# Kernel optimization log

Hardware: AMD Instinct MI355X
Metric: run time of the kernel (lower is better)

## Reference

```python
import jax, jax.numpy as jnp
import numpy as np

N = 100000       # nodes
E = 1600000      # edges
F_IN = 128       # num_node_features
H = 256          # graph_hidden_channels
NHID = 512
NOUT = 256
G = 256          # graphs in batch


def setup_inputs() -> dict:
    key = jax.random.key(0)
    ks = jax.random.split(key, 14)
    x = jax.random.normal(ks[0], (N, F_IN), jnp.float32)
    src = jax.random.randint(ks[1], (E,), 0, N, jnp.int32)
    dst = jax.random.randint(ks[2], (E,), 0, N, jnp.int32)
    batch = jnp.sort(jax.random.randint(ks[3], (N,), 0, G, jnp.int32))
    def lin(k, fan_in, fan_out):
        return jax.random.normal(k, (fan_in, fan_out), jnp.float32) * (1.0 / np.sqrt(fan_in))
    return {
        "x": x, "src": src, "dst": dst, "batch": batch,
        "W1": lin(ks[4], F_IN, H), "b1": jnp.zeros((H,), jnp.float32),
        "W2": lin(ks[5], H, H),    "b2": jnp.zeros((H,), jnp.float32),
        "W3": lin(ks[6], H, H),    "b3": jnp.zeros((H,), jnp.float32),
        "Wm1": lin(ks[7], H, NHID), "bm1": jnp.zeros((NHID,), jnp.float32),
        "Wm2": lin(ks[8], NHID, NOUT), "bm2": jnp.zeros((NOUT,), jnp.float32),
    }


def _gcn_layer(h_in, W, b, src, dst, dinv):
    # GCNConv: transform, then symmetric-normalized aggregation with self-loops.
    h = h_in @ W                                            # [N, out]
    norm = (dinv[src] * dinv[dst])[:, None]                 # [E, 1]
    agg = jax.ops.segment_sum(h[src] * norm, dst, num_segments=N)
    agg = agg + h * (dinv * dinv)[:, None]                  # self-loop term (norm = 1/deg)
    return agg + b


def reference(x, src, dst, batch, W1, b1, W2, b2, W3, b3, Wm1, bm1, Wm2, bm2):
    # degrees include the added self-loop (+1)
    deg = 1.0 + jax.ops.segment_sum(jnp.ones((E,), x.dtype), dst, num_segments=N)
    dinv = jax.lax.rsqrt(deg)                               # deg^{-1/2}

    h = jax.nn.relu(_gcn_layer(x, W1, b1, src, dst, dinv))
    h = jax.nn.relu(_gcn_layer(h, W2, b2, src, dst, dinv))
    h = _gcn_layer(h, W3, b3, src, dst, dinv)               # no relu before pooling

    # global mean pool over graphs
    counts = jax.ops.segment_sum(jnp.ones((N,), x.dtype), batch, num_segments=G)
    pooled = jax.ops.segment_sum(h, batch, num_segments=G) / jnp.maximum(counts, 1.0)[:, None]

    out = jax.nn.relu(pooled @ Wm1 + bm1) @ Wm2 + bm2       # [G, NOUT]
    return out
```

## Files before the change

kernel.cpp:

```cpp
#include <hip/hip_runtime.h>
#include <hip/hip_bf16.h>

#define N_NODES 100000
#define N_EDGES 1600000
#define F_IN    128
#define H       256
#define NHID    512
#define NOUT    256
#define G_GR    256

typedef unsigned short u16;
typedef __attribute__((ext_vector_type(8))) short s16x8;
typedef __attribute__((ext_vector_type(8))) unsigned short u16x8;
typedef __attribute__((ext_vector_type(4))) float f32x4;

__device__ __forceinline__ float bf2f(u16 u) {
    union { unsigned int i; float f; } v; v.i = ((unsigned int)u) << 16; return v.f;
}
__device__ __forceinline__ u16 f2bf(float f) {
    union { float f; unsigned int i; } v; v.f = f;
    unsigned int x = v.i;
    x += 0x7fffu + ((x >> 16) & 1u);
    return (u16)(x >> 16);
}

#define CD_BLKS   1563
#define SPX_BLKS  ((N_NODES * F_IN) / 1024)
#define T1_BLKS   ((F_IN * H) / 256)
#define T2_BLKS   ((H * H) / 256)
#define T3_BLKS   ((H * H) / 256)
#define TM1_BLKS  ((H * NHID) / 256)
#define TM2_BLKS  ((NHID * NOUT) / 256)
#define HEAD_BLKS (CD_BLKS + SPX_BLKS + T1_BLKS + T2_BLKS + T3_BLKS + TM1_BLKS + TM2_BLKS + 2)

__device__ __forceinline__ void transpose_split_body(const float* __restrict__ W,
        u16* __restrict__ thi, u16* __restrict__ tlo, int K, int N, int id) {
    int n = id / K, k = id - n * K;
    float f = W[(size_t)k * N + n];
    u16 h = f2bf(f);
    thi[id] = h;
    tlo[id] = f2bf(f - bf2f(h));
}

__global__ __launch_bounds__(256) void prep_head(
        const int* __restrict__ dst, int* __restrict__ degc,
        const float* __restrict__ x, u16* __restrict__ x_bf,
        const float* __restrict__ W1, u16* __restrict__ t1h, u16* __restrict__ t1l,
        const float* __restrict__ W2, u16* __restrict__ t2h, u16* __restrict__ t2l,
        const float* __restrict__ W3, u16* __restrict__ t3h, u16* __restrict__ t3l,
        const float* __restrict__ Wm1, u16* __restrict__ tm1h, u16* __restrict__ tm1l,
        const float* __restrict__ Wm2, u16* __restrict__ tm2h, u16* __restrict__ tm2l,
        const int* __restrict__ batch, int* __restrict__ goff) {
    int bid = blockIdx.x;
    if (bid < CD_BLKS) {
        int base = bid * 1024 + threadIdx.x;
#pragma unroll
        for (int q = 0; q < 4; q++) {
            int e = base + q * 256;
            if (e < N_EDGES) atomicAdd(&degc[dst[e]], 1);
        }
        return;
    }
    bid -= CD_BLKS;
    if (bid < SPX_BLKS) {
        int idx = bid * 256 + threadIdx.x;
        float4 f = *(const float4*)&x[(size_t)idx * 4];
        ushort4 o;
        o.x = f2bf(f.x); o.y = f2bf(f.y); o.z = f2bf(f.z); o.w = f2bf(f.w);
        *(ushort4*)&x_bf[(size_t)idx * 4] = o;
        return;
    }
    bid -= SPX_BLKS;
    if (bid < T1_BLKS) {
        transpose_split_body(W1, t1h, t1l, F_IN, H, bid * 256 + threadIdx.x);
        return;
    }
    bid -= T1_BLKS;
    if (bid < T2_BLKS) {
        transpose_split_body(W2, t2h, t2l, H, H, bid * 256 + threadIdx.x);
        return;
    }
    bid -= T2_BLKS;
    if (bid < T3_BLKS) {
        transpose_split_body(W3, t3h, t3l, H, H, bid * 256 + threadIdx.x);
        return;
    }
    bid -= T3_BLKS;
    if (bid < TM1_BLKS) {
        transpose_split_body(Wm1, tm1h, tm1l, H, NHID, bid * 256 + threadIdx.x);
        return;
    }
    bid -= TM1_BLKS;
    if (bid < TM2_BLKS) {
        transpose_split_body(Wm2, tm2h, tm2l, NHID, NOUT, bid * 256 + threadIdx.x);
        return;
    }
    bid -= TM2_BLKS;
    {
        int g = bid * 256 + threadIdx.x;
        if (g > G_GR) return;
        int lo = 0, hi = N_NODES;
        while (lo < hi) {
            int mid = (lo + hi) >> 1;
            if (batch[mid] < g) lo = mid + 1; else hi = mid;
        }
        goff[g] = lo;
    }
}

__global__ void scan_partial(const int* __restrict__ cnt, int* __restrict__ partial) {
    __shared__ int s[256];
    int t = threadIdx.x;
    int i = blockIdx.x * 256 + t;
    int v = (i < N_NODES) ? cnt[i] : 0;
    s[t] = v; __syncthreads();
    for (int off = 128; off > 0; off >>= 1) {
        if (t < off) s[t] += s[t + off];
        __syncthreads();
    }
    if (t == 0) partial[blockIdx.x] = s[0];
}

__global__ void scan_offsets(int* __restrict__ partial, int nb, int* __restrict__ rowp) {
    __shared__ int s[512];
    int t = threadIdx.x;
    int orig = (t < nb) ? partial[t] : 0;
    s[t] = orig; __syncthreads();
    for (int off = 1; off < 512; off <<= 1) {
        int u = (t >= off) ? s[t - off] : 0;
        __syncthreads();
        s[t] += u;
        __syncthreads();
    }
    if (t < nb) partial[t] = s[t] - orig;
    if (t == 0) rowp[N_NODES] = N_EDGES;
}

__global__ void scan_final_dinv(const int* __restrict__ cnt, const int* __restrict__ partial,
                                int* __restrict__ rowp, int* __restrict__ cur,
                                float* __restrict__ dinv) {
    __shared__ int s[256];
    int t = threadIdx.x;
    int i = blockIdx.x * 256 + t;
    int v = (i < N_NODES) ? cnt[i] : 0;
    s[t] = v; __syncthreads();
    for (int off = 1; off < 256; off <<= 1) {
        int u = (t >= off) ? s[t - off] : 0;
        __syncthreads();
        s[t] += u;
        __syncthreads();
    }
    if (i < N_NODES) {
        int r = partial[blockIdx.x] + s[t] - v;
        rowp[i] = r;
        cur[i] = r;
        dinv[i] = rsqrtf(1.0f + (float)v);
    }
}

__global__ __launch_bounds__(256) void scatter_edges(
        const int* __restrict__ src, const int* __restrict__ dst,
        const float* __restrict__ dinv, int* __restrict__ cur,
        int2* __restrict__ ep) {
    int base = blockIdx.x * 1024 + threadIdx.x;
#pragma unroll
    for (int q = 0; q < 4; q++) {
        int e = base + q * 256;
        if (e < N_EDGES) {
            int d = dst[e];
            int s = src[e];
            float w = dinv[d] * dinv[s];
            int pos = atomicAdd(&cur[d], 1);
            int2 v; v.x = s; v.y = __float_as_int(w);
            ep[pos] = v;
        }
    }
}

__global__ __launch_bounds__(256) void gcn_agg256(
        const u16* __restrict__ in, const int* __restrict__ rowp,
        const int2* __restrict__ ep, const float* __restrict__ dinv,
        u16* __restrict__ outp) {
    int node = blockIdx.x * 8 + (threadIdx.x >> 5);
    int l = threadIdx.x & 31;
    int beg = rowp[node], end = rowp[node + 1];
    float a[8] = {};
    int e = beg;
    int2 pr[8];
    bool have = (e + 8 <= end);
    if (have) {
#pragma unroll
        for (int q = 0; q < 8; q++) pr[q] = ep[e + q];
    }
    while (have) {
        int2 g8[8];
#pragma unroll
        for (int q = 0; q < 8; q++) g8[q] = pr[q];
        int en = e + 8;
        bool haven = (en + 8 <= end);
        if (haven) {
#pragma unroll
            for (int q = 0; q < 8; q++) pr[q] = ep[en + q];
        }
#pragma unroll
        for (int q = 0; q < 8; q++) {
            u16x8 u = *(const u16x8*)&in[(size_t)g8[q].x * H + l * 8];
            float wt = __int_as_float(g8[q].y);
#pragma unroll
            for (int r = 0; r < 8; r++) a[r] += bf2f(u[r]) * wt;
        }
        e = en; have = haven;
    }
    for (; e < end; e++) {
        int2 pe = ep[e];
        float wt = __int_as_float(pe.y);
        u16x8 u = *(const u16x8*)&in[(size_t)pe.x * H + l * 8];
#pragma unroll
        for (int r = 0; r < 8; r++) a[r] += bf2f(u[r]) * wt;
    }
    float di = dinv[node];
    u16x8 us = *(const u16x8*)&in[(size_t)node * H + l * 8];
    float dd = di * di;
    u16x8 o;
#pragma unroll
    for (int r = 0; r < 8; r++) o[r] = f2bf(a[r] + bf2f(us[r]) * dd);
    *(u16x8*)&outp[(size_t)node * H + l * 8] = o;
}

__global__ __launch_bounds__(256) void gcn_agg128(
        const u16* __restrict__ in, const int* __restrict__ rowp,
        const int2* __restrict__ ep, const float* __restrict__ dinv,
        u16* __restrict__ outp) {
    int node = blockIdx.x * 16 + (threadIdx.x >> 4);
    int l = threadIdx.x & 15;
    int beg = rowp[node], end = rowp[node + 1];
    float a[8] = {};
    int e = beg;
    int2 pr[8];
    bool have = (e + 8 <= end);
    if (have) {
#pragma unroll
        for (int q = 0; q < 8; q++) pr[q] = ep[e + q];
    }
    while (have) {
        int2 g8[8];
#pragma unroll
        for (int q = 0; q < 8; q++) g8[q] = pr[q];
        int en = e + 8;
        bool haven = (en + 8 <= end);
        if (haven) {
#pragma unroll
            for (int q = 0; q < 8; q++) pr[q] = ep[en + q];
        }
#pragma unroll
        for (int q = 0; q < 8; q++) {
            u16x8 u = *(const u16x8*)&in[(size_t)g8[q].x * F_IN + l * 8];
            float wt = __int_as_float(g8[q].y);
#pragma unroll
            for (int r = 0; r < 8; r++) a[r] += bf2f(u[r]) * wt;
        }
        e = en; have = haven;
    }
    for (; e < end; e++) {
        int2 pe = ep[e];
        float wt = __int_as_float(pe.y);
        u16x8 u = *(const u16x8*)&in[(size_t)pe.x * F_IN + l * 8];
#pragma unroll
        for (int r = 0; r < 8; r++) a[r] += bf2f(u[r]) * wt;
    }
    float di = dinv[node];
    u16x8 us = *(const u16x8*)&in[(size_t)node * F_IN + l * 8];
    float dd = di * di;
    u16x8 o;
#pragma unroll
    for (int r = 0; r < 8; r++) o[r] = f2bf(a[r] + bf2f(us[r]) * dd);
    *(u16x8*)&outp[(size_t)node * F_IN + l * 8] = o;
}

template<int K, bool RELU>
__global__ __launch_bounds__(256) void gemm_bias(
        const u16* __restrict__ A,
        const u16* __restrict__ Bhi, const u16* __restrict__ Blo,
        const float* __restrict__ bias, u16* __restrict__ C, int M) {
    __shared__ __align__(16) u16 sA[128 * 40];
    __shared__ __align__(16) u16 sB[2 * 128 * 40];
    const int tid = threadIdx.x;
    const int w = tid >> 6, l = tid & 63;
    const int wm = (w & 1) * 64, wn = (w >> 1) * 64;
    const int bm = blockIdx.x * 128, bn = blockIdx.y * 128;
    const int srow = tid >> 2;
    const int schunk = (tid & 3) * 8;
    const int lr = l & 15, lg = (l >> 4) * 8;

    f32x4 acc[4][4] = {};

    for (int k0 = 0; k0 < K; k0 += 32) {
        {
            int r0 = bm + srow, r1 = bm + srow + 64;
            u16x8 v0 = {}, v1 = {};
            if (r0 < M) v0 = *(const u16x8*)&A[(size_t)r0 * K + k0 + schunk];
            if (r1 < M) v1 = *(const u16x8*)&A[(size_t)r1 * K + k0 + schunk];
            *(u16x8*)&sA[srow * 40 + schunk] = v0;
            *(u16x8*)&sA[(srow + 64) * 40 + schunk] = v1;
        }
        {
            int n0 = bn + srow, n1 = bn + srow + 64;
            *(u16x8*)&sB[srow * 40 + schunk] = *(const u16x8*)&Bhi[(size_t)n0 * K + k0 + schunk];
            *(u16x8*)&sB[(srow + 64) * 40 + schunk] = *(const u16x8*)&Bhi[(size_t)n1 * K + k0 + schunk];
            *(u16x8*)&sB[128 * 40 + srow * 40 + schunk] = *(const u16x8*)&Blo[(size_t)n0 * K + k0 + schunk];
            *(u16x8*)&sB[128 * 40 + (srow + 64) * 40 + schunk] = *(const u16x8*)&Blo[(size_t)n1 * K + k0 + schunk];
        }
        __syncthreads();

        s16x8 af[4], bh[4], bl[4];
#pragma unroll
        for (int i = 0; i < 4; i++)
            af[i] = __builtin_bit_cast(s16x8, *(const u16x8*)&sA[(wm + i * 16 + lr) * 40 + lg]);
#pragma unroll
        for (int j = 0; j < 4; j++) {
            bh[j] = __builtin_bit_cast(s16x8, *(const u16x8*)&sB[(wn + j * 16 + lr) * 40 + lg]);
            bl[j] = __builtin_bit_cast(s16x8, *(const u16x8*)&sB[128 * 40 + (wn + j * 16 + lr) * 40 + lg]);
        }
#pragma unroll
        for (int i = 0; i < 4; i++) {
#pragma unroll
            for (int j = 0; j < 4; j++) {
                acc[i][j] = __builtin_amdgcn_mfma_f32_16x16x32_bf16(af[i], bh[j], acc[i][j], 0, 0, 0);
                acc[i][j] = __builtin_amdgcn_mfma_f32_16x16x32_bf16(af[i], bl[j], acc[i][j], 0, 0, 0);
            }
        }
        __syncthreads();
    }

    float bcol[4];
#pragma unroll
    for (int j = 0; j < 4; j++) bcol[j] = bias[bn + wn + j * 16 + lr];

    const int lq = (l >> 4) * 4;
#pragma unroll
    for (int i = 0; i < 4; i++) {
#pragma unroll
        for (int r0 = 0; r0 < 4; r0++) {
            int row = bm + wm + i * 16 + lq + r0;
            if (row < M) {
#pragma unroll
                for (int j = 0; j < 4; j++) {
                    float v = acc[i][j][r0] + bcol[j];
                    if (RELU) v = fmaxf(v, 0.f);
                    C[(size_t)row * H + bn + wn + j * 16 + lr] = f2bf(v);
                }
            }
        }
    }
}

template<int K, int NW, bool RELU, bool F32OUT>
__global__ __launch_bounds__(256) void gemm_split(
        const u16* __restrict__ Ahi, const u16* __restrict__ Alo,
        const u16* __restrict__ Bhi, const u16* __restrict__ Blo,
        const float* __restrict__ bias,
        u16* __restrict__ Chi, u16* __restrict__ Clo, float* __restrict__ Cf,
        int M) {
    __shared__ __align__(16) u16 sA[2 * 128 * 40];
    __shared__ __align__(16) u16 sB[2 * 128 * 40];
    const int tid = threadIdx.x;
    const int w = tid >> 6, l = tid & 63;
    const int wm = (w & 1) * 64, wn = (w >> 1) * 64;
    const int bm = blockIdx.x * 128, bn = blockIdx.y * 128;
    const int srow = tid >> 2;
    const int schunk = (tid & 3) * 8;
    const int lr = l & 15, lg = (l >> 4) * 8;

    f32x4 acc[4][4] = {};

    for (int k0 = 0; k0 < K; k0 += 32) {
        {
            int r0 = bm + srow, r1 = bm + srow + 64;
            u16x8 v0 = {}, v1 = {}, w0 = {}, w1 = {};
            if (r0 < M) {
                v0 = *(const u16x8*)&Ahi[(size_t)r0 * K + k0 + schunk];
                w0 = *(const u16x8*)&Alo[(size_t)r0 * K + k0 + schunk];
            }
            if (r1 < M) {
                v1 = *(const u16x8*)&Ahi[(size_t)r1 * K + k0 + schunk];
                w1 = *(const u16x8*)&Alo[(size_t)r1 * K + k0 + schunk];
            }
            *(u16x8*)&sA[srow * 40 + schunk] = v0;
            *(u16x8*)&sA[(srow + 64) * 40 + schunk] = v1;
            *(u16x8*)&sA[128 * 40 + srow * 40 + schunk] = w0;
            *(u16x8*)&sA[128 * 40 + (srow + 64) * 40 + schunk] = w1;
        }
        {
            int n0 = bn + srow, n1 = bn + srow + 64;
            *(u16x8*)&sB[srow * 40 + schunk] = *(const u16x8*)&Bhi[(size_t)n0 * K + k0 + schunk];
            *(u16x8*)&sB[(srow + 64) * 40 + schunk] = *(const u16x8*)&Bhi[(size_t)n1 * K + k0 + schunk];
            *(u16x8*)&sB[128 * 40 + srow * 40 + schunk] = *(const u16x8*)&Blo[(size_t)n0 * K + k0 + schunk];
            *(u16x8*)&sB[128 * 40 + (srow + 64) * 40 + schunk] = *(const u16x8*)&Blo[(size_t)n1 * K + k0 + schunk];
        }
        __syncthreads();

        s16x8 af[4], al[4], bh[4], bl[4];
#pragma unroll
        for (int i = 0; i < 4; i++) {
            af[i] = __builtin_bit_cast(s16x8, *(const u16x8*)&sA[(wm + i * 16 + lr) * 40 + lg]);
            al[i] = __builtin_bit_cast(s16x8, *(const u16x8*)&sA[128 * 40 + (wm + i * 16 + lr) * 40 + lg]);
        }
#pragma unroll
        for (int j = 0; j < 4; j++) {
            bh[j] = __builtin_bit_cast(s16x8, *(const u16x8*)&sB[(wn + j * 16 + lr) * 40 + lg]);
            bl[j] = __builtin_bit_cast(s16x8, *(const u16x8*)&sB[128 * 40 + (wn + j * 16 + lr) * 40 + lg]);
        }
#pragma unroll
        for (int i = 0; i < 4; i++) {
#pragma unroll
            for (int j = 0; j < 4; j++) {
                acc[i][j] = __builtin_amdgcn_mfma_f32_16x16x32_bf16(af[i], bh[j], acc[i][j], 0, 0, 0);
                acc[i][j] = __builtin_amdgcn_mfma_f32_16x16x32_bf16(af[i], bl[j], acc[i][j], 0, 0, 0);
                acc[i][j] = __builtin_amdgcn_mfma_f32_16x16x32_bf16(al[i], bh[j], acc[i][j], 0, 0, 0);
            }
        }
        __syncthreads();
    }

    float bcol[4];
#pragma unroll
    for (int j = 0; j < 4; j++) bcol[j] = bias[bn + wn + j * 16 + lr];

    const int lq = (l >> 4) * 4;
#pragma unroll
    for (int i = 0; i < 4; i++) {
#pragma unroll
        for (int r0 = 0; r0 < 4; r0++) {
            int row = bm + wm + i * 16 + lq + r0;
            if (row < M) {
#pragma unroll
                for (int j = 0; j < 4; j++) {
                    float v = acc[i][j][r0] + bcol[j];
                    if (RELU) v = fmaxf(v, 0.f);
                    size_t idx = (size_t)row * NW + bn + wn + j * 16 + lr;
                    if (F32OUT) {
                        Cf[idx] = v;
                    } else {
                        u16 hv = f2bf(v);
                        Chi[idx] = hv;
                        Clo[idx] = f2bf(v - bf2f(hv));
                    }
                }
            }
        }
    }
}

__global__ __launch_bounds__(256) void pool_split(
        const u16* __restrict__ a3, const int* __restrict__ goff,
        u16* __restrict__ phi, u16* __restrict__ plo) {
    int g = blockIdx.x, t = threadIdx.x;
    int beg = goff[g], end = goff[g + 1];
    float acc = 0.f;
    int i = beg;
    for (; i + 4 <= end; i += 4) {
        float v0 = bf2f(a3[(size_t)(i + 0) * H + t]);
        float v1 = bf2f(a3[(size_t)(i + 1) * H + t]);
        float v2 = bf2f(a3[(size_t)(i + 2) * H + t]);
        float v3 = bf2f(a3[(size_t)(i + 3) * H + t]);
        acc += (v0 + v1) + (v2 + v3);
    }
    for (; i < end; i++) acc += bf2f(a3[(size_t)i * H + t]);
    acc /= fmaxf((float)(end - beg), 1.f);
    u16 hv = f2bf(acc);
    phi[g * H + t] = hv;
    plo[g * H + t] = f2bf(acc - bf2f(hv));
}

extern "C" void kernel_launch(void* const* d_in, const int* in_sizes, int n_in,
                              void* d_out, int out_size, void* d_ws, size_t ws_size,
                              hipStream_t stream) {
    const float* x   = (const float*)d_in[0];
    const int*   src = (const int*)d_in[1];
    const int*   dst = (const int*)d_in[2];
    const int*   bat = (const int*)d_in[3];
    const float* W1  = (const float*)d_in[4];  const float* b1  = (const float*)d_in[5];
    const float* W2  = (const float*)d_in[6];  const float* b2  = (const float*)d_in[7];
    const float* W3  = (const float*)d_in[8];  const float* b3  = (const float*)d_in[9];
    const float* Wm1 = (const float*)d_in[10]; const float* bm1 = (const float*)d_in[11];
    const float* Wm2 = (const float*)d_in[12]; const float* bm2 = (const float*)d_in[13];
    float* out = (float*)d_out;

    char* p = (char*)d_ws;
    auto carve = [&](size_t bytes) -> void* {
        void* r = (void*)p;
        p += (bytes + 511) & ~(size_t)511;
        return r;
    };
    u16*   x_bf    = (u16*)  carve((size_t)N_NODES * F_IN * 2);
    u16*   aggX    = (u16*)  carve((size_t)N_NODES * F_IN * 2);
    u16*   bufA    = (u16*)  carve((size_t)N_NODES * H * 2);
    u16*   bufB    = (u16*)  carve((size_t)N_NODES * H * 2);
    float* dinv    = (float*)carve((size_t)N_NODES * 4);
    int*   degc    = (int*)  carve((size_t)N_NODES * 4);
    int*   rowp    = (int*)  carve((size_t)(N_NODES + 1) * 4);
    int*   cur     = (int*)  carve((size_t)N_NODES * 4);
    int2*  ep      = (int2*) carve((size_t)N_EDGES * 8);
    int*   partial = (int*)  carve(4096);
    int*   goff    = (int*)  carve((size_t)(G_GR + 1) * 4);
    u16*   Wt1_hi  = (u16*)  carve((size_t)F_IN * H * 2);
    u16*   Wt1_lo  = (u16*)  carve((size_t)F_IN * H * 2);
    u16*   Wt2_hi  = (u16*)  carve((size_t)H * H * 2);
    u16*   Wt2_lo  = (u16*)  carve((size_t)H * H * 2);
    u16*   Wt3_hi  = (u16*)  carve((size_t)H * H * 2);
    u16*   Wt3_lo  = (u16*)  carve((size_t)H * H * 2);
    u16*   Wm1t_hi = (u16*)  carve((size_t)H * NHID * 2);
    u16*   Wm1t_lo = (u16*)  carve((size_t)H * NHID * 2);
    u16*   Wm2t_hi = (u16*)  carve((size_t)NHID * NOUT * 2);
    u16*   Wm2t_lo = (u16*)  carve((size_t)NHID * NOUT * 2);
    u16*   p_hi    = (u16*)  carve((size_t)G_GR * H * 2);
    u16*   p_lo    = (u16*)  carve((size_t)G_GR * H * 2);
    u16*   y_hi    = (u16*)  carve((size_t)G_GR * H * 2);
    u16*   y_lo    = (u16*)  carve((size_t)G_GR * H * 2);
    u16*   hd_hi   = (u16*)  carve((size_t)G_GR * NHID * 2);
    u16*   hd_lo   = (u16*)  carve((size_t)G_GR * NHID * 2);

    const int NB = (N_NODES + 255) / 256;

    hipMemsetAsync(degc, 0, (size_t)N_NODES * 4, stream);
    prep_head<<<HEAD_BLKS, 256, 0, stream>>>(dst, degc, x, x_bf,
                                             W1, Wt1_hi, Wt1_lo,
                                             W2, Wt2_hi, Wt2_lo,
                                             W3, Wt3_hi, Wt3_lo,
                                             Wm1, Wm1t_hi, Wm1t_lo,
                                             Wm2, Wm2t_hi, Wm2t_lo, bat, goff);
    scan_partial<<<NB, 256, 0, stream>>>(degc, partial);
    scan_offsets<<<1, 512, 0, stream>>>(partial, NB, rowp);
    scan_final_dinv<<<NB, 256, 0, stream>>>(degc, partial, rowp, cur, dinv);
    scatter_edges<<<CD_BLKS, 256, 0, stream>>>(src, dst, dinv, cur, ep);

    dim3 ggrid((N_NODES + 127) / 128, 2);

    gcn_agg128<<<N_NODES / 16, 256, 0, stream>>>(x_bf, rowp, ep, dinv, aggX);
    gemm_bias<F_IN, true><<<ggrid, 256, 0, stream>>>(aggX, Wt1_hi, Wt1_lo, b1, bufA, N_NODES);
    gcn_agg256<<<N_NODES / 8, 256, 0, stream>>>(bufA, rowp, ep, dinv, bufB);
    gemm_bias<H, true><<<ggrid, 256, 0, stream>>>(bufB, Wt2_hi, Wt2_lo, b2, bufA, N_NODES);
    gcn_agg256<<<N_NODES / 8, 256, 0, stream>>>(bufA, rowp, ep, dinv, bufB);

    pool_split<<<G_GR, 256, 0, stream>>>(bufB, goff, p_hi, p_lo);
    dim3 g3(2, 2), gm1(2, 4), gm2(2, 2);
    gemm_split<H, H, false, false><<<g3, 256, 0, stream>>>(
        p_hi, p_lo, Wt3_hi, Wt3_lo, b3, y_hi, y_lo, nullptr, G_GR);
    gemm_split<H, NHID, true, false><<<gm1, 256, 0, stream>>>(
        y_hi, y_lo, Wm1t_hi, Wm1t_lo, bm1, hd_hi, hd_lo, nullptr, G_GR);
    gemm_split<NHID, NOUT, false, true><<<gm2, 256, 0, stream>>>(
        hd_hi, hd_lo, Wm2t_hi, Wm2t_lo, bm2, nullptr, nullptr, out, G_GR);
}
```

Baseline: 752.1 us.

## Widen GEMM tile to full 256 columns with 512 threads; nontemporal edge stores

The node GEMM now uses 512-thread blocks that each compute a 128x256 output tile covering all columns. The A tile is loaded once per block instead of once for each of two column blocks, which halves A global reads and drops the second grid dimension. The edge scatter now packs each (src, weight) pair into one 64-bit value and writes it with a nontemporal store to reduce cache pollution. The larger LDS footprint and block size may lower occupancy.

Measured after the change: 763.8 us. No clear change (+1.6%).

```diff
diff --git a/kernel.cpp b/kernel.cpp
--- a/kernel.cpp
+++ b/kernel.cpp
@@ -161,7 +161,7 @@
 __global__ __launch_bounds__(256) void scatter_edges(
         const int* __restrict__ src, const int* __restrict__ dst,
         const float* __restrict__ dinv, int* __restrict__ cur,
-        int2* __restrict__ ep) {
+        long long* __restrict__ ep) {
     int base = blockIdx.x * 1024 + threadIdx.x;
 #pragma unroll
     for (int q = 0; q < 4; q++) {
@@ -171,8 +171,8 @@
             int s = src[e];
             float w = dinv[d] * dinv[s];
             int pos = atomicAdd(&cur[d], 1);
-            int2 v; v.x = s; v.y = __float_as_int(w);
-            ep[pos] = v;
+            long long v = ((long long)__float_as_int(w) << 32) | (unsigned int)s;
+            __builtin_nontemporal_store(v, &ep[pos]);
         }
     }
 }
@@ -278,16 +278,17 @@
 }
 
 template<int K, bool RELU>
-__global__ __launch_bounds__(256) void gemm_bias(
+__global__ __launch_bounds__(512) void gemm_bias(
         const u16* __restrict__ A,
         const u16* __restrict__ Bhi, const u16* __restrict__ Blo,
         const float* __restrict__ bias, u16* __restrict__ C, int M) {
     __shared__ __align__(16) u16 sA[128 * 40];
-    __shared__ __align__(16) u16 sB[2 * 128 * 40];
+    __shared__ __align__(16) u16 sBh[256 * 40];
+    __shared__ __align__(16) u16 sBl[256 * 40];
     const int tid = threadIdx.x;
     const int w = tid >> 6, l = tid & 63;
-    const int wm = (w & 1) * 64, wn = (w >> 1) * 64;
-    const int bm = blockIdx.x * 128, bn = blockIdx.y * 128;
+    const int wm = (w >> 2) * 64, wn = (w & 3) * 64;
+    const int bm = blockIdx.x * 128;
     const int srow = tid >> 2;
     const int schunk = (tid & 3) * 8;
     const int lr = l & 15, lg = (l >> 4) * 8;
@@ -296,19 +297,17 @@
 
     for (int k0 = 0; k0 < K; k0 += 32) {
         {
-            int r0 = bm + srow, r1 = bm + srow + 64;
-            u16x8 v0 = {}, v1 = {};
+            int r0 = bm + srow;
+            u16x8 v0 = {};
             if (r0 < M) v0 = *(const u16x8*)&A[(size_t)r0 * K + k0 + schunk];
-            if (r1 < M) v1 = *(const u16x8*)&A[(size_t)r1 * K + k0 + schunk];
             *(u16x8*)&sA[srow * 40 + schunk] = v0;
-            *(u16x8*)&sA[(srow + 64) * 40 + schunk] = v1;
         }
         {
-            int n0 = bn + srow, n1 = bn + srow + 64;
-            *(u16x8*)&sB[srow * 40 + schunk] = *(const u16x8*)&Bhi[(size_t)n0 * K + k0 + schunk];
-            *(u16x8*)&sB[(srow + 64) * 40 + schunk] = *(const u16x8*)&Bhi[(size_t)n1 * K + k0 + schunk];
-            *(u16x8*)&sB[128 * 40 + srow * 40 + schunk] = *(const u16x8*)&Blo[(size_t)n0 * K + k0 + schunk];
-            *(u16x8*)&sB[128 * 40 + (srow + 64) * 40 + schunk] = *(const u16x8*)&Blo[(size_t)n1 * K + k0 + schunk];
+            int n0 = srow, n1 = srow + 128;
+            *(u16x8*)&sBh[n0 * 40 + schunk] = *(const u16x8*)&Bhi[(size_t)n0 * K + k0 + schunk];
+            *(u16x8*)&sBh[n1 * 40 + schunk] = *(const u16x8*)&Bhi[(size_t)n1 * K + k0 + schunk];
+            *(u16x8*)&sBl[n0 * 40 + schunk] = *(const u16x8*)&Blo[(size_t)n0 * K + k0 + schunk];
+            *(u16x8*)&sBl[n1 * 40 + schunk] = *(const u16x8*)&Blo[(size_t)n1 * K + k0 + schunk];
         }
         __syncthreads();
 
@@ -318,8 +317,8 @@
             af[i] = __builtin_bit_cast(s16x8, *(const u16x8*)&sA[(wm + i * 16 + lr) * 40 + lg]);
 #pragma unroll
         for (int j = 0; j < 4; j++) {
-            bh[j] = __builtin_bit_cast(s16x8, *(const u16x8*)&sB[(wn + j * 16 + lr) * 40 + lg]);
-            bl[j] = __builtin_bit_cast(s16x8, *(const u16x8*)&sB[128 * 40 + (wn + j * 16 + lr) * 40 + lg]);
+            bh[j] = __builtin_bit_cast(s16x8, *(const u16x8*)&sBh[(wn + j * 16 + lr) * 40 + lg]);
+            bl[j] = __builtin_bit_cast(s16x8, *(const u16x8*)&sBl[(wn + j * 16 + lr) * 40 + lg]);
         }
 #pragma unroll
         for (int i = 0; i < 4; i++) {
@@ -334,7 +333,7 @@
 
     float bcol[4];
 #pragma unroll
-    for (int j = 0; j < 4; j++) bcol[j] = bias[bn + wn + j * 16 + lr];
+    for (int j = 0; j < 4; j++) bcol[j] = bias[wn + j * 16 + lr];
 
     const int lq = (l >> 4) * 4;
 #pragma unroll
@@ -347,7 +346,7 @@
                 for (int j = 0; j < 4; j++) {
                     float v = acc[i][j][r0] + bcol[j];
                     if (RELU) v = fmaxf(v, 0.f);
-                    C[(size_t)row * H + bn + wn + j * 16 + lr] = f2bf(v);
+                    C[(size_t)row * H + wn + j * 16 + lr] = f2bf(v);
                 }
             }
         }
@@ -532,14 +531,14 @@
     scan_partial<<<NB, 256, 0, stream>>>(degc, partial);
     scan_offsets<<<1, 512, 0, stream>>>(partial, NB, rowp);
     scan_final_dinv<<<NB, 256, 0, stream>>>(degc, partial, rowp, cur, dinv);
-    scatter_edges<<<CD_BLKS, 256, 0, stream>>>(src, dst, dinv, cur, ep);
-
-    dim3 ggrid((N_NODES + 127) / 128, 2);
+    scatter_edges<<<CD_BLKS, 256, 0, stream>>>(src, dst, dinv, cur, (long long*)ep);
+
+    const int GB = (N_NODES + 127) / 128;
 
     gcn_agg128<<<N_NODES / 16, 256, 0, stream>>>(x_bf, rowp, ep, dinv, aggX);
-    gemm_bias<F_IN, true><<<ggrid, 256, 0, stream>>>(aggX, Wt1_hi, Wt1_lo, b1, bufA, N_NODES);
+    gemm_bias<F_IN, true><<<GB, 512, 0, stream>>>(aggX, Wt1_hi, Wt1_lo, b1, bufA, N_NODES);
     gcn_agg256<<<N_NODES / 8, 256, 0, stream>>>(bufA, rowp, ep, dinv, bufB);
-    gemm_bias<H, true><<<ggrid, 256, 0, stream>>>(bufB, Wt2_hi, Wt2_lo, b2, bufA, N_NODES);
+    gemm_bias<H, true><<<GB, 512, 0, stream>>>(bufB, Wt2_hi, Wt2_lo, b2, bufA, N_NODES);
     gcn_agg256<<<N_NODES / 8, 256, 0, stream>>>(bufA, rowp, ep, dinv, bufB);
 
     pool_split<<<G_GR, 256, 0, stream>>>(bufB, goff, p_hi, p_lo);
```

## Two-pass bucketed edge scatter to localize CSR build writes

Applied to the files above, without the earlier changes.

Replaces the single random scatter of edges into CSR order with two passes. The first pass places each edge into a coarse bucket of 512 destination nodes using a per-bucket atomic counter, and records the local destination index. The second pass reads each bucket contiguously and scatters edges to their final positions within a small address window. The aim is better write locality and less atomic contention, at the cost of an extra staging buffer, an extra kernel launch, and more total memory traffic. The 196 bucket counters in the first pass are heavily contended atomics.

After: 1.607 ms. +113.6%, slower.

```diff
diff --git a/kernel.cpp b/kernel.cpp
--- a/kernel.cpp
+++ b/kernel.cpp
@@ -8,6 +8,7 @@
 #define NHID    512
 #define NOUT    256
 #define G_GR    256
+#define NBUCK   196
 
 typedef unsigned short u16;
 typedef __attribute__((ext_vector_type(8))) short s16x8;
@@ -138,7 +139,7 @@
 
 __global__ void scan_final_dinv(const int* __restrict__ cnt, const int* __restrict__ partial,
                                 int* __restrict__ rowp, int* __restrict__ cur,
-                                float* __restrict__ dinv) {
+                                int* __restrict__ bcur, float* __restrict__ dinv) {
     __shared__ int s[256];
     int t = threadIdx.x;
     int i = blockIdx.x * 256 + t;
@@ -154,14 +155,15 @@
         int r = partial[blockIdx.x] + s[t] - v;
         rowp[i] = r;
         cur[i] = r;
+        if ((i & 511) == 0) bcur[i >> 9] = r;
         dinv[i] = rsqrtf(1.0f + (float)v);
     }
 }
 
-__global__ __launch_bounds__(256) void scatter_edges(
+__global__ __launch_bounds__(256) void scatter_bucket(
         const int* __restrict__ src, const int* __restrict__ dst,
-        const float* __restrict__ dinv, int* __restrict__ cur,
-        int2* __restrict__ ep) {
+        const float* __restrict__ dinv, int* __restrict__ bcur,
+        int2* __restrict__ ep_stage, u16* __restrict__ dloc) {
     int base = blockIdx.x * 1024 + threadIdx.x;
 #pragma unroll
     for (int q = 0; q < 4; q++) {
@@ -170,10 +172,30 @@
             int d = dst[e];
             int s = src[e];
             float w = dinv[d] * dinv[s];
-            int pos = atomicAdd(&cur[d], 1);
+            int b = d >> 9;
+            int pos = atomicAdd(&bcur[b], 1);
             int2 v; v.x = s; v.y = __float_as_int(w);
-            ep[pos] = v;
-        }
+            ep_stage[pos] = v;
+            dloc[pos] = (u16)(d & 511);
+        }
+    }
+}
+
+__global__ __launch_bounds__(256) void scatter_final(
+        const int* __restrict__ rowp, int* __restrict__ cur,
+        const int2* __restrict__ ep_stage, const u16* __restrict__ dloc,
+        int2* __restrict__ ep) {
+    int b = blockIdx.x >> 2;
+    int quarter = blockIdx.x & 3;
+    int nodeBase = b << 9;
+    int beg = rowp[nodeBase];
+    int endn = nodeBase + 512; if (endn > N_NODES) endn = N_NODES;
+    int end = rowp[endn];
+    for (int p = beg + quarter * 256 + threadIdx.x; p < end; p += 1024) {
+        int2 v = ep_stage[p];
+        int d = nodeBase + dloc[p];
+        int q = atomicAdd(&cur[d], 1);
+        ep[q] = v;
     }
 }
 
@@ -500,7 +522,10 @@
     int*   degc    = (int*)  carve((size_t)N_NODES * 4);
     int*   rowp    = (int*)  carve((size_t)(N_NODES + 1) * 4);
     int*   cur     = (int*)  carve((size_t)N_NODES * 4);
+    int*   bcur    = (int*)  carve((size_t)NBUCK * 4);
     int2*  ep      = (int2*) carve((size_t)N_EDGES * 8);
+    int2*  ep_stage= (int2*) carve((size_t)N_EDGES * 8);
+    u16*   dloc    = (u16*)  carve((size_t)N_EDGES * 2);
     int*   partial = (int*)  carve(4096);
     int*   goff    = (int*)  carve((size_t)(G_GR + 1) * 4);
     u16*   Wt1_hi  = (u16*)  carve((size_t)F_IN * H * 2);
@@ -531,8 +556,9 @@
                                              Wm2, Wm2t_hi, Wm2t_lo, bat, goff);
     scan_partial<<<NB, 256, 0, stream>>>(degc, partial);
     scan_offsets<<<1, 512, 0, stream>>>(partial, NB, rowp);
-    scan_final_dinv<<<NB, 256, 0, stream>>>(degc, partial, rowp, cur, dinv);
-    scatter_edges<<<CD_BLKS, 256, 0, stream>>>(src, dst, dinv, cur, ep);
+    scan_final_dinv<<<NB, 256, 0, stream>>>(degc, partial, rowp, cur, bcur, dinv);
+    scatter_bucket<<<CD_BLKS, 256, 0, stream>>>(src, dst, dinv, bcur, ep_stage, dloc);
+    scatter_final<<<NBUCK * 4, 256, 0, stream>>>(rowp, cur, ep_stage, dloc, ep);
 
     dim3 ggrid((N_NODES + 127) / 128, 2);
 
```
